# Kernel optimization log

Measured on AMD Instinct MI355X. Metric: run time of the kernel, lower is better.

Reference implementation:

```python
import jax, jax.numpy as jnp
import numpy as np

V, D, NH, T_MAX, L, MLP = 50257, 1024, 16, 1024, 12, 4
HD = D // NH
F = D * MLP
B, T = 2, 1024


def setup_inputs() -> dict:
    key = jax.random.key(0)
    ks = jax.random.split(key, 16)
    s = 0.02
    inp = {
        'tokens': jax.random.randint(ks[0], (B, T), 0, V, dtype=jnp.int32),
        'wte': jax.random.normal(ks[1], (V, D), jnp.float32) * s,
        'wpe': jax.random.normal(ks[2], (T_MAX, D), jnp.float32) * s,
        'ln1_w': jnp.ones((L, D)), 'ln1_b': jnp.zeros((L, D)),
        'attn_w': jax.random.normal(ks[3], (L, D, 3 * D), jnp.float32) * s,
        'attn_b': jnp.zeros((L, 3 * D)),
        'aproj_w': jax.random.normal(ks[4], (L, D, D), jnp.float32) * s,
        'aproj_b': jnp.zeros((L, D)),
        'ln2_w': jnp.ones((L, D)), 'ln2_b': jnp.zeros((L, D)),
        'fc_w': jax.random.normal(ks[5], (L, D, F), jnp.float32) * s,
        'fc_b': jnp.zeros((L, F)),
        'proj_w': jax.random.normal(ks[6], (L, F, D), jnp.float32) * s,
        'proj_b': jnp.zeros((L, D)),
        'lnf_w': jnp.ones((D,)), 'lnf_b': jnp.zeros((D,)),
    }
    return inp


def _ln(x, w, b, eps=1e-5):
    m = jnp.mean(x, -1, keepdims=True)
    v = jnp.var(x, -1, keepdims=True)
    return (x - m) * jax.lax.rsqrt(v + eps) * w + b


def _forward(tokens, wte, wpe, ln1_w, ln1_b, attn_w, attn_b, aproj_w, aproj_b,
             ln2_w, ln2_b, fc_w, fc_b, proj_w, proj_b, lnf_w, lnf_b):
    b, t = tokens.shape
    x = wte[tokens] + wpe[:t]  # [B,T,D]
    scale = HD ** -0.5
    causal = jnp.tril(jnp.ones((t, t), bool))  # [T,T]

    def block(x, p):
        l1w, l1b, aw, ab, apw, apb, l2w, l2b, fw, fb, pw, pb = p
        h = _ln(x, l1w, l1b)
        qkv = h @ aw + ab  # [B,T,3D]
        q, k, v = jnp.split(qkv, 3, axis=-1)
        # rearrange 'b t (h n) -> b n t h' with n=NH: last dim is (head_size, n_heads)
        def split_heads(u):
            return u.reshape(b, t, HD, NH).transpose(0, 3, 1, 2)  # [B,NH,T,HD]
        q, k, v = split_heads(q), split_heads(k), split_heads(v)
        scores = jnp.einsum('bnth,bnsh->bnts', q, k) * scale
        scores = jnp.where(causal, scores, -jnp.inf)
        w = jax.nn.softmax(scores, axis=-1)
        att = jnp.einsum('bnts,bnsh->bnth', w, v)
        # rearrange 'b n t h -> b t (n h)'
        att = att.transpose(0, 2, 1, 3).reshape(b, t, D)
        x = x + (att @ apw + apb)
        h2 = _ln(x, l2w, l2b)
        x = x + (jax.nn.gelu(h2 @ fw + fb, approximate=False) @ pw + pb)
        return x, None

    params = (ln1_w, ln1_b, attn_w, attn_b, aproj_w, aproj_b,
              ln2_w, ln2_b, fc_w, fc_b, proj_w, proj_b)
    x, _ = jax.lax.scan(block, x, params)
    x = _ln(x, lnf_w, lnf_b)[:, -1:, :]  # [B,1,D]
    return x @ wte.T  # tied lm_head -> [B,1,V]


def reference(tokens, wte, wpe, ln1_w, ln1_b, attn_w, attn_b, aproj_w, aproj_b,
              ln2_w, ln2_b, fc_w, fc_b, proj_w, proj_b, lnf_w, lnf_b):
    return _forward(tokens, wte, wpe, ln1_w, ln1_b, attn_w, attn_b, aproj_w,
                    aproj_b, ln2_w, ln2_b, fc_w, fc_b, proj_w, proj_b, lnf_w, lnf_b)
```

## Files before the change

### kernel.cpp

```cpp
#include <hip/hip_runtime.h>
#include <cstdint>
#include <math.h>


using u16 = unsigned short;
using bf16x8 = __attribute__((ext_vector_type(8))) short;
using f32x4 = __attribute__((ext_vector_type(4))) float;

#define GLDS16(g, l)                                                        \
  __builtin_amdgcn_global_load_lds(                                         \
      (const __attribute__((address_space(1))) void*)(g),                   \
      (__attribute__((address_space(3))) void*)(l), 16, 0, 0)

__device__ __forceinline__ u16 f2bf(float f) {
  union { float f; unsigned u; } t; t.f = f;
  unsigned r = t.u + 0x7fffu + ((t.u >> 16) & 1u);
  return (u16)(r >> 16);
}

__device__ __forceinline__ float fast_erf(float x) {
  float ax = fabsf(x);
  float t = 1.f / (1.f + 0.3275911f * ax);
  float y = t * (0.254829592f +
            t * (-0.284496736f +
            t * (1.421413741f +
            t * (-1.453152027f +
            t * 1.061405429f))));
  float r = 1.f - y * __expf(-ax * ax);
  return copysignf(r, x);
}

#define DD 1024
#define TTT 1024
#define MR 2048
#define FFF 4096
#define VVV 50257

__global__ __launch_bounds__(256) void k_embed(const int* __restrict__ tokens,
                                               const float* __restrict__ wte,
                                               const float* __restrict__ wpe,
                                               float* __restrict__ x) {
  int m = blockIdx.x, d = threadIdx.x * 4;
  int t = m & (TTT - 1);
  int tok = tokens[m];
  const float4 a = *(const float4*)(wte + (size_t)tok * DD + d);
  const float4 p = *(const float4*)(wpe + (size_t)t * DD + d);
  float4 o; o.x = a.x + p.x; o.y = a.y + p.y; o.z = a.z + p.z; o.w = a.w + p.w;
  *(float4*)(x + (size_t)m * DD + d) = o;
}

__device__ __forceinline__ void addln_body(float* __restrict__ x,
                                           const float* __restrict__ pp, int npart,
                                           const float* __restrict__ w,
                                           const float* __restrict__ b,
                                           u16* __restrict__ out, int blk) {
  const int wid = threadIdx.x >> 6, lane = threadIdx.x & 63;
  const int m = blk * 4 + wid;
  float* row = x + (size_t)m * DD;
  float4 v[4];
  float s = 0.f, q = 0.f;
#pragma unroll
  for (int j = 0; j < 4; ++j) {
    v[j] = *(const float4*)(row + j * 256 + lane * 4);
    for (int p = 0; p < npart; ++p) {
      const float4 pv = *(const float4*)(pp + (size_t)p * MR * DD + (size_t)m * DD + j * 256 + lane * 4);
      v[j].x += pv.x; v[j].y += pv.y; v[j].z += pv.z; v[j].w += pv.w;
    }
    if (npart) *(float4*)(row + j * 256 + lane * 4) = v[j];
    s += v[j].x + v[j].y + v[j].z + v[j].w;
    q += v[j].x * v[j].x + v[j].y * v[j].y + v[j].z * v[j].z + v[j].w * v[j].w;
  }
#pragma unroll
  for (int off = 1; off < 64; off <<= 1) { s += __shfl_xor(s, off); q += __shfl_xor(q, off); }
  float mean = s * (1.f / DD);
  float var = q * (1.f / DD) - mean * mean;
  float rs = rsqrtf(var + 1e-5f);
#pragma unroll
  for (int j = 0; j < 4; ++j) {
    const float4 wv = *(const float4*)(w + j * 256 + lane * 4);
    const float4 bv = *(const float4*)(b + j * 256 + lane * 4);
    u16 o[4];
    o[0] = f2bf((v[j].x - mean) * rs * wv.x + bv.x);
    o[1] = f2bf((v[j].y - mean) * rs * wv.y + bv.y);
    o[2] = f2bf((v[j].z - mean) * rs * wv.z + bv.z);
    o[3] = f2bf((v[j].w - mean) * rs * wv.w + bv.w);
    *(uint64_t*)(out + (size_t)m * DD + j * 256 + lane * 4) = *(uint64_t*)o;
  }
}

__global__ __launch_bounds__(256) void k_addln(float* __restrict__ x,
                                               const float* __restrict__ pp, int npart,
                                               const float* __restrict__ w,
                                               const float* __restrict__ b,
                                               u16* __restrict__ out) {
  addln_body(x, pp, npart, w, b, out, blockIdx.x);
}

__device__ __forceinline__ void wtrans_body(const float* __restrict__ atw,
                                            const float* __restrict__ apw,
                                            const float* __restrict__ fcw,
                                            const float* __restrict__ pjw,
                                            u16* __restrict__ wt, int id) {
  __shared__ u16 tb[64][72];
  const float* W; u16* Wt; int K, N, local, kts; bool perm = false;
  if (id < 768)       { W = atw; Wt = wt;           K = 1024; N = 3072; local = id;        kts = 4; perm = true; }
  else if (id < 1024) { W = apw; Wt = wt + 3145728; K = 1024; N = 1024; local = id - 768;  kts = 4; }
  else if (id < 2048) { W = fcw; Wt = wt + 4194304; K = 1024; N = 4096; local = id - 1024; kts = 4; }
  else                { W = pjw; Wt = wt + 8388608; K = 4096; N = 1024; local = id - 2048; kts = 6; }
  const int k0 = (local & ((1 << kts) - 1)) * 64, n0 = (local >> kts) * 64;
  const int tid = threadIdx.x;
  const int rr = tid >> 4, c4 = (tid & 15) * 4;
#pragma unroll
  for (int i = 0; i < 4; ++i) {
    const int r = rr + i * 16;
    const float4 v = *(const float4*)(W + (size_t)(k0 + r) * N + n0 + c4);
    tb[c4 + 0][r] = f2bf(v.x);
    tb[c4 + 1][r] = f2bf(v.y);
    tb[c4 + 2][r] = f2bf(v.z);
    tb[c4 + 3][r] = f2bf(v.w);
  }
  __syncthreads();
  const int n = tid >> 3, k8 = (tid & 7) * 8;
#pragma unroll
  for (int s = 0; s < 2; ++s) {
    u16 o[8];
#pragma unroll
    for (int j = 0; j < 8; ++j) o[j] = tb[n + s * 32][k8 + j];
    int orow = n0 + n + s * 32;
    if (perm) {
      int part = orow >> 10, w = orow & 1023;
      orow = part * 1024 + (w & 15) * 64 + (w >> 4);
    }
    *(bf16x8*)(Wt + (size_t)orow * K + k0 + k8) = *(bf16x8*)o;
  }
}

__global__ __launch_bounds__(256) void k_prep(float* __restrict__ x,
                                              const float* __restrict__ pp, int npart,
                                              const float* __restrict__ w,
                                              const float* __restrict__ b,
                                              u16* __restrict__ out,
                                              const float* __restrict__ atw,
                                              const float* __restrict__ apw,
                                              const float* __restrict__ fcw,
                                              const float* __restrict__ pjw,
                                              u16* __restrict__ wt,
                                              const float* __restrict__ ab,
                                              float* __restrict__ pbias) {
  if (blockIdx.x < 512) {
    addln_body(x, pp, npart, w, b, out, blockIdx.x);
  } else if (blockIdx.x == 3584) {
    for (int c = threadIdx.x; c < 3072; c += 256) {
      int part = c >> 10, ww = c & 1023;
      pbias[c] = ab[part * 1024 + (ww & 63) * 16 + (ww >> 6)];
    }
  } else {
    wtrans_body(atw, apw, fcw, pjw, wt, blockIdx.x - 512);
  }
}

template <int EPI>
__global__ __launch_bounds__(256) void k_gemm(const u16* __restrict__ A,
                                              const u16* __restrict__ Bt,
                                              const float* __restrict__ bias,
                                              u16* __restrict__ outb,
                                              float* __restrict__ pp,
                                              int M, int N, int K, int KC) {
  __shared__ u16 As[2][128 * 64];
  __shared__ u16 Bs[2][128 * 64];
  const int nbx = gridDim.x, nby = gridDim.y;
  const int nwg = nbx * nby * gridDim.z;
  const int orig = blockIdx.x + nbx * (blockIdx.y + nby * blockIdx.z);
  const int qq = nwg >> 3, rr = nwg & 7;
  const int xcd = orig & 7, pos = orig >> 3;
  const int wg = (xcd < rr ? xcd * (qq + 1) : rr * (qq + 1) + (xcd - rr) * qq) + pos;
  const int bx = wg % nbx;
  const int tmpw = wg / nbx;
  const int by = tmpw % nby, bz = tmpw / nby;

  const int tid = threadIdx.x;
  const int lane = tid & 63, wid = tid >> 6;
  const int wr = wid >> 1, wc = wid & 1;
  const int l15 = lane & 15, l4 = lane >> 4;
  const int sx = l15 & 7;
  const int m0 = bx * 128, n0 = by * 128;
  f32x4 acc[4][4] = {};

  const int srow = tid >> 3;
  const int scol = (((tid & 7) ^ (srow & 7)) * 8);
  const int k0beg = bz * KC;
  const int nt = KC >> 6;

  const u16* Ap = A + (size_t)(m0 + srow) * K + scol;
  const u16* Bp = Bt + (size_t)(n0 + srow) * K + scol;

#define STAGE(buf, k0)                                                      \
  {                                                                         \
    _Pragma("unroll")                                                       \
    for (int it = 0; it < 4; ++it) {                                        \
      GLDS16(Ap + (size_t)it * 32 * K + (k0), (char*)As[buf] + it * 4096 + tid * 16); \
      GLDS16(Bp + (size_t)it * 32 * K + (k0), (char*)Bs[buf] + it * 4096 + tid * 16); \
    }                                                                       \
  }

  STAGE(0, k0beg);
  for (int t = 0; t < nt; ++t) {
    if (t + 1 < nt) {
      STAGE((t + 1) & 1, k0beg + (t + 1) * 64);
      asm volatile("s_waitcnt vmcnt(8)" ::: "memory");
    } else {
      asm volatile("s_waitcnt vmcnt(0)" ::: "memory");
    }
    __builtin_amdgcn_sched_barrier(0);
    __builtin_amdgcn_s_barrier();
    __builtin_amdgcn_sched_barrier(0);
    const u16* Ab = As[t & 1];
    const u16* Bb = Bs[t & 1];
#pragma unroll
    for (int ks = 0; ks < 2; ++ks) {
      const int ch = ((ks * 4 + l4) ^ sx) * 8;
      bf16x8 af[4], bfr[4];
#pragma unroll
      for (int i = 0; i < 4; ++i)
        af[i] = *(const bf16x8*)(Ab + (wr * 64 + i * 16 + l15) * 64 + ch);
#pragma unroll
      for (int j = 0; j < 4; ++j)
        bfr[j] = *(const bf16x8*)(Bb + (wc * 64 + j * 16 + l15) * 64 + ch);
      __builtin_amdgcn_s_setprio(1);
#pragma unroll
      for (int i = 0; i < 4; ++i)
#pragma unroll
        for (int j = 0; j < 4; ++j)
          acc[i][j] = __builtin_amdgcn_mfma_f32_16x16x32_bf16(af[i], bfr[j], acc[i][j], 0, 0, 0);
      __builtin_amdgcn_s_setprio(0);
    }
    __builtin_amdgcn_sched_barrier(0);
    __builtin_amdgcn_s_barrier();
    __builtin_amdgcn_sched_barrier(0);
  }
#undef STAGE
  float* ppz = (EPI == 4) ? pp + (size_t)bz * M * N : nullptr;
#pragma unroll
  for (int j = 0; j < 4; ++j) {
    const int col = n0 + wc * 64 + j * 16 + l15;
    const float bs = (EPI == 4 && bz != 0) ? 0.f : bias[col];
#pragma unroll
    for (int i = 0; i < 4; ++i) {
#pragma unroll
      for (int r = 0; r < 4; ++r) {
        const int row = m0 + wr * 64 + i * 16 + l4 * 4 + r;
        float v = acc[i][j][r] + bs;
        if (EPI == 0) {
          outb[(size_t)row * N + col] = f2bf(v);
        } else if (EPI == 2) {
          float g = 0.5f * v * (1.f + fast_erf(v * 0.70710678118f));
          outb[(size_t)row * N + col] = f2bf(g);
        } else {
          ppz[(size_t)row * N + col] = v;
        }
      }
    }
  }
}

__global__ __launch_bounds__(256) void k_repack(const u16* __restrict__ qkv,
                                                u16* __restrict__ Vt) {
  __shared__ u16 tile[16][1032];
  const int tid = threadIdx.x;
  const int m0 = blockIdx.x * 16;
  const int b = m0 >> 10;
  const int tg0 = m0 & (TTT - 1);
#pragma unroll
  for (int p = 0; p < 8; ++p) {
    int row = p * 2 + (tid >> 7);
    int col8 = (tid & 127) * 8;
    bf16x8 v = *(const bf16x8*)(qkv + (size_t)(m0 + row) * 3072 + 2048 + col8);
    *(bf16x8*)(&tile[row][col8]) = v;
  }
  __syncthreads();
  const int lane = tid & 63, wid = tid >> 6;
  for (int p = wid; p < 32; p += 4) {
    int n = p >> 1, tc = p & 1;
    u16 o[8];
#pragma unroll
    for (int k = 0; k < 8; ++k) o[k] = tile[tc * 8 + k][n * 64 + lane];
    *(bf16x8*)(Vt + (((size_t)(b * 16 + n)) * 64 + lane) * TTT + tg0 + tc * 8) =
        *(bf16x8*)o;
  }
}

__global__ __launch_bounds__(256) void k_attn(const u16* __restrict__ qkv,
                                              const u16* __restrict__ Vt,
                                              u16* __restrict__ attout) {
  __shared__ u16 Ks[128 * 64];
  __shared__ u16 Vs[64 * 128];
  __shared__ u16 Ps[4][16 * 136];

  const int tid = threadIdx.x;
  const int lane = tid & 63, wid = tid >> 6;
  const int l15 = lane & 15, l4 = lane >> 4;
  const int bn = blockIdx.x;
  const int b = bn >> 4, nh = bn & 15;
  const char* Kg0 = (const char*)(qkv + (size_t)b * TTT * 3072 + 1024 + nh * 64);
  const char* Vg0 = (const char*)(Vt + (size_t)bn * 64 * TTT);

#pragma unroll
  for (int pass = 0; pass < 2; ++pass) {
    const int qtr = pass == 0 ? 15 - (int)blockIdx.y : (int)blockIdx.y;
    const int q0 = qtr * 64;

    const int qrow = q0 + wid * 16 + l15;
    const u16* qsrc = qkv + (size_t)(b * TTT + qrow) * 3072 + nh * 64;
    bf16x8 aq[2];
#pragma unroll
    for (int ks = 0; ks < 2; ++ks)
      aq[ks] = *(const bf16x8*)(qsrc + ks * 32 + l4 * 8);

    float m_run[4], l_part[4];
    f32x4 o[4] = {};
#pragma unroll
    for (int r = 0; r < 4; ++r) { m_run[r] = -1e30f; l_part[r] = 0.f; }

    const int ntk = (qtr >> 1) + 1;
    for (int kt = 0; kt < ntk; ++kt) {
#pragma unroll
      for (int it = 0; it < 4; ++it) {
        int L = it * 4096 + tid * 16;
        int Ls = L ^ (((L >> 7) & 7) << 4);
        int krow = Ls >> 7, cb = Ls & 127;
        GLDS16(Kg0 + (size_t)(kt * 128 + krow) * 6144 + cb, (char*)Ks + L);
      }
#pragma unroll
      for (int it = 0; it < 4; ++it) {
        int L = it * 4096 + tid * 16;
        int Ls = L ^ (((L >> 8) & 7) << 4);
        int hrow = Ls >> 8, cb = Ls & 255;
        GLDS16(Vg0 + (size_t)hrow * 2048 + kt * 256 + cb, (char*)Vs + L);
      }
      __syncthreads();

      f32x4 sf[8];
#pragma unroll
      for (int cf = 0; cf < 8; ++cf) {
        f32x4 z = {};
#pragma unroll
        for (int ks = 0; ks < 2; ++ks) {
          int P = (cf * 16 + l15) * 128 + (ks * 32 + l4 * 8) * 2;
          bf16x8 kb = *(const bf16x8*)((const char*)Ks + (P ^ (((P >> 7) & 7) << 4)));
          z = __builtin_amdgcn_mfma_f32_16x16x32_bf16(aq[ks], kb, z, 0, 0, 0);
        }
        sf[cf] = z;
      }
      const bool lastkt = (kt == ntk - 1);
#pragma unroll
      for (int cf = 0; cf < 8; ++cf)
#pragma unroll
        for (int r = 0; r < 4; ++r) {
          float s = sf[cf][r] * 0.125f;
          if (lastkt) {
            int kg = kt * 128 + cf * 16 + l15;
            int qg = q0 + wid * 16 + l4 * 4 + r;
            if (kg > qg) s = -1e30f;
          }
          sf[cf][r] = s;
        }
      float fac[4];
#pragma unroll
      for (int r = 0; r < 4; ++r) {
        float tm = sf[0][r];
#pragma unroll
        for (int cf = 1; cf < 8; ++cf) tm = fmaxf(tm, sf[cf][r]);
#pragma unroll
        for (int off = 1; off < 16; off <<= 1) tm = fmaxf(tm, __shfl_xor(tm, off));
        float mnew = fmaxf(m_run[r], tm);
        fac[r] = __expf(m_run[r] - mnew);
        m_run[r] = mnew;
        float ps = 0.f;
#pragma unroll
        for (int cf = 0; cf < 8; ++cf) {
          float p = __expf(sf[cf][r] - mnew);
          sf[cf][r] = p;
          ps += p;
        }
        l_part[r] = l_part[r] * fac[r] + ps;
      }
#pragma unroll
      for (int cf = 0; cf < 8; ++cf)
#pragma unroll
        for (int r = 0; r < 4; ++r)
          Ps[wid][(l4 * 4 + r) * 136 + cf * 16 + l15] = f2bf(sf[cf][r]);
#pragma unroll
      for (int hf = 0; hf < 4; ++hf)
#pragma unroll
        for (int r = 0; r < 4; ++r) o[hf][r] *= fac[r];
      bf16x8 pa[4];
#pragma unroll
      for (int ks = 0; ks < 4; ++ks)
        pa[ks] = *(const bf16x8*)&Ps[wid][l15 * 136 + ks * 32 + l4 * 8];
#pragma unroll
      for (int hf = 0; hf < 4; ++hf) {
#pragma unroll
        for (int ks = 0; ks < 4; ++ks) {
          int P = (hf * 16 + l15) * 256 + (ks * 32 + l4 * 8) * 2;
          bf16x8 vb = *(const bf16x8*)((const char*)Vs + (P ^ (((P >> 8) & 7) << 4)));
          o[hf] = __builtin_amdgcn_mfma_f32_16x16x32_bf16(pa[ks], vb, o[hf], 0, 0, 0);
        }
      }
      __syncthreads();
    }
    float lsum[4];
#pragma unroll
    for (int r = 0; r < 4; ++r) {
      float s = l_part[r];
#pragma unroll
      for (int off = 1; off < 16; off <<= 1) s += __shfl_xor(s, off);
      lsum[r] = s;
    }
#pragma unroll
    for (int hf = 0; hf < 4; ++hf)
#pragma unroll
      for (int r = 0; r < 4; ++r) {
        float val = o[hf][r] / lsum[r];
        size_t row = (size_t)b * TTT + q0 + wid * 16 + l4 * 4 + r;
        attout[row * DD + nh * 64 + hf * 16 + l15] = f2bf(val);
      }
  }
}

__global__ __launch_bounds__(256) void k_head(const float* __restrict__ x,
                                              const float* __restrict__ pp, int npart,
                                              const float* __restrict__ lnf_w,
                                              const float* __restrict__ lnf_b,
                                              const float* __restrict__ wte,
                                              float* __restrict__ out) {
  __shared__ float xs[2 * DD];
  __shared__ float sm[8];
  int tid = threadIdx.x;
  int wid = tid >> 6, lane = tid & 63;
#pragma unroll
  for (int bb = 0; bb < 2; ++bb) {
    int m = bb * TTT + (TTT - 1);
    float4 v = *(const float4*)(x + (size_t)m * DD + tid * 4);
    for (int p = 0; p < npart; ++p) {
      const float4 pv = *(const float4*)(pp + (size_t)p * MR * DD + (size_t)m * DD + tid * 4);
      v.x += pv.x; v.y += pv.y; v.z += pv.z; v.w += pv.w;
    }
    float s = v.x + v.y + v.z + v.w;
    float q = v.x * v.x + v.y * v.y + v.z * v.z + v.w * v.w;
#pragma unroll
    for (int off = 1; off < 64; off <<= 1) { s += __shfl_xor(s, off); q += __shfl_xor(q, off); }
    if ((tid & 63) == 0) { sm[wid] = s; sm[4 + wid] = q; }
    __syncthreads();
    s = sm[0] + sm[1] + sm[2] + sm[3];
    q = sm[4] + sm[5] + sm[6] + sm[7];
    float mean = s * (1.f / DD);
    float var = q * (1.f / DD) - mean * mean;
    float rs = rsqrtf(var + 1e-5f);
    const float4 wv = *(const float4*)(lnf_w + tid * 4);
    const float4 bv = *(const float4*)(lnf_b + tid * 4);
    float4 o;
    o.x = (v.x - mean) * rs * wv.x + bv.x;
    o.y = (v.y - mean) * rs * wv.y + bv.y;
    o.z = (v.z - mean) * rs * wv.z + bv.z;
    o.w = (v.w - mean) * rs * wv.w + bv.w;
    *(float4*)(xs + bb * DD + tid * 4) = o;
    __syncthreads();
  }
  for (int v = blockIdx.x * 4 + wid; v < VVV; v += gridDim.x * 4) {
    const float* wr = wte + (size_t)v * DD;
    float a0 = 0.f, a1 = 0.f;
#pragma unroll
    for (int j = 0; j < 4; ++j) {
      const float4 wv = *(const float4*)(wr + lane * 16 + j * 4);
      const float4 x0 = *(const float4*)(xs + lane * 16 + j * 4);
      const float4 x1 = *(const float4*)(xs + DD + lane * 16 + j * 4);
      a0 += wv.x * x0.x + wv.y * x0.y + wv.z * x0.z + wv.w * x0.w;
      a1 += wv.x * x1.x + wv.y * x1.y + wv.z * x1.z + wv.w * x1.w;
    }
#pragma unroll
    for (int off = 1; off < 64; off <<= 1) { a0 += __shfl_xor(a0, off); a1 += __shfl_xor(a1, off); }
    if (lane == 0) { out[v] = a0; out[VVV + v] = a1; }
  }
}

extern "C" void kernel_launch(void* const* d_in, const int* in_sizes, int n_in,
                              void* d_out, int out_size, void* d_ws, size_t ws_size,
                              hipStream_t stream) {
  const int* tokens    = (const int*)d_in[0];
  const float* wte     = (const float*)d_in[1];
  const float* wpe     = (const float*)d_in[2];
  const float* ln1_w   = (const float*)d_in[3];
  const float* ln1_b   = (const float*)d_in[4];
  const float* attn_w  = (const float*)d_in[5];
  const float* attn_b  = (const float*)d_in[6];
  const float* aproj_w = (const float*)d_in[7];
  const float* aproj_b = (const float*)d_in[8];
  const float* ln2_w   = (const float*)d_in[9];
  const float* ln2_b   = (const float*)d_in[10];
  const float* fc_w    = (const float*)d_in[11];
  const float* fc_b    = (const float*)d_in[12];
  const float* proj_w  = (const float*)d_in[13];
  const float* proj_b  = (const float*)d_in[14];
  const float* lnf_w   = (const float*)d_in[15];
  const float* lnf_b   = (const float*)d_in[16];

  char* ws = (char*)d_ws;
  float* x    = (float*)(ws);
  u16* h      = (u16*)(ws + (8u << 20));
  u16* wt     = (u16*)(ws + (12u << 20));
  u16* qkv    = (u16*)(ws + (36u << 20));
  u16* Vt     = (u16*)(ws + (52u << 20));
  u16* attb   = (u16*)(ws + (56u << 20));
  u16* mlph   = (u16*)(ws + (36u << 20));
  float* pp   = (float*)(ws + (60u << 20));
  float* pbias = (float*)(ws + (92u << 20));
  float* out  = (float*)d_out;

  u16* atw = wt;
  u16* apw = wt + 3145728;
  u16* fcw = wt + 4194304;
  u16* pjw = wt + 8388608;

  k_embed<<<MR, 256, 0, stream>>>(tokens, wte, wpe, x);

  for (int l = 0; l < 12; ++l) {
    k_prep<<<3585, 256, 0, stream>>>(x, pp, l == 0 ? 0 : 4,
                                     ln1_w + l * DD, ln1_b + l * DD, h,
                                     attn_w + (size_t)l * DD * 3 * DD,
                                     aproj_w + (size_t)l * DD * DD,
                                     fc_w + (size_t)l * DD * FFF,
                                     proj_w + (size_t)l * FFF * DD, wt,
                                     attn_b + (size_t)l * 3 * DD, pbias);
    k_gemm<0><<<dim3(16, 24, 1), 256, 0, stream>>>(h, atw, pbias, qkv, nullptr, MR, 3072, 1024, 1024);
    k_repack<<<128, 256, 0, stream>>>(qkv, Vt);
    k_attn<<<dim3(32, 8), 256, 0, stream>>>(qkv, Vt, attb);
    k_gemm<4><<<dim3(16, 8, 2), 256, 0, stream>>>(attb, apw, aproj_b + (size_t)l * DD, nullptr, pp, MR, 1024, 1024, 512);
    k_addln<<<512, 256, 0, stream>>>(x, pp, 2, ln2_w + l * DD, ln2_b + l * DD, h);
    k_gemm<2><<<dim3(16, 32, 1), 256, 0, stream>>>(h, fcw, fc_b + (size_t)l * FFF, mlph, nullptr, MR, 4096, 1024, 1024);
    k_gemm<4><<<dim3(16, 8, 4), 256, 0, stream>>>(mlph, pjw, proj_b + (size_t)l * DD, nullptr, pp, MR, 1024, 4096, 1024);
  }
  k_head<<<512, 256, 0, stream>>>(x, pp, 4, lnf_w, lnf_b, wte, out);
}
```

Before: 1.857 ms.

## Stage GEMM epilogue through LDS, store split-K partials as bf16

The GEMM epilogue now writes results into shared memory and then emits coalesced 16-byte row stores, replacing scattered per-element global writes. Split-K partial sums are stored as bf16 instead of fp32, halving partial-buffer traffic in the GEMM and the add+layernorm consumers. The attention projection is split four ways instead of two. Storing partials in bf16 loses precision in the residual accumulation, and the extra split adds partial traffic.

```diff
diff --git a/kernel.cpp b/kernel.cpp
--- a/kernel.cpp
+++ b/kernel.cpp
@@ -16,6 +16,10 @@
   union { float f; unsigned u; } t; t.f = f;
   unsigned r = t.u + 0x7fffu + ((t.u >> 16) & 1u);
   return (u16)(r >> 16);
+}
+__device__ __forceinline__ float bf2f(u16 v) {
+  union { unsigned u; float f; } t; t.u = ((unsigned)v) << 16;
+  return t.f;
 }
 
 __device__ __forceinline__ float fast_erf(float x) {
@@ -50,7 +54,7 @@
 }
 
 __device__ __forceinline__ void addln_body(float* __restrict__ x,
-                                           const float* __restrict__ pp, int npart,
+                                           const u16* __restrict__ pp, int npart,
                                            const float* __restrict__ w,
                                            const float* __restrict__ b,
                                            u16* __restrict__ out, int blk) {
@@ -62,9 +66,13 @@
 #pragma unroll
   for (int j = 0; j < 4; ++j) {
     v[j] = *(const float4*)(row + j * 256 + lane * 4);
+#pragma unroll 4
     for (int p = 0; p < npart; ++p) {
-      const float4 pv = *(const float4*)(pp + (size_t)p * MR * DD + (size_t)m * DD + j * 256 + lane * 4);
-      v[j].x += pv.x; v[j].y += pv.y; v[j].z += pv.z; v[j].w += pv.w;
+      uint64_t pv = *(const uint64_t*)(pp + (size_t)p * MR * DD + (size_t)m * DD + j * 256 + lane * 4);
+      v[j].x += bf2f((u16)(pv));
+      v[j].y += bf2f((u16)(pv >> 16));
+      v[j].z += bf2f((u16)(pv >> 32));
+      v[j].w += bf2f((u16)(pv >> 48));
     }
     if (npart) *(float4*)(row + j * 256 + lane * 4) = v[j];
     s += v[j].x + v[j].y + v[j].z + v[j].w;
@@ -89,7 +97,7 @@
 }
 
 __global__ __launch_bounds__(256) void k_addln(float* __restrict__ x,
-                                               const float* __restrict__ pp, int npart,
+                                               const u16* __restrict__ pp, int npart,
                                                const float* __restrict__ w,
                                                const float* __restrict__ b,
                                                u16* __restrict__ out) {
@@ -136,7 +144,7 @@
 }
 
 __global__ __launch_bounds__(256) void k_prep(float* __restrict__ x,
-                                              const float* __restrict__ pp, int npart,
+                                              const u16* __restrict__ pp, int npart,
                                               const float* __restrict__ w,
                                               const float* __restrict__ b,
                                               u16* __restrict__ out,
@@ -164,10 +172,9 @@
                                               const u16* __restrict__ Bt,
                                               const float* __restrict__ bias,
                                               u16* __restrict__ outb,
-                                              float* __restrict__ pp,
+                                              u16* __restrict__ pp,
                                               int M, int N, int K, int KC) {
-  __shared__ u16 As[2][128 * 64];
-  __shared__ u16 Bs[2][128 * 64];
+  __shared__ u16 smem[4][128 * 64];
   const int nbx = gridDim.x, nby = gridDim.y;
   const int nwg = nbx * nby * gridDim.z;
   const int orig = blockIdx.x + nbx * (blockIdx.y + nby * blockIdx.z);
@@ -198,8 +205,8 @@
   {                                                                         \
     _Pragma("unroll")                                                       \
     for (int it = 0; it < 4; ++it) {                                        \
-      GLDS16(Ap + (size_t)it * 32 * K + (k0), (char*)As[buf] + it * 4096 + tid * 16); \
-      GLDS16(Bp + (size_t)it * 32 * K + (k0), (char*)Bs[buf] + it * 4096 + tid * 16); \
+      GLDS16(Ap + (size_t)it * 32 * K + (k0), (char*)smem[buf] + it * 4096 + tid * 16); \
+      GLDS16(Bp + (size_t)it * 32 * K + (k0), (char*)smem[2 + (buf)] + it * 4096 + tid * 16); \
     }                                                                       \
   }
 
@@ -214,8 +221,8 @@
     __builtin_amdgcn_sched_barrier(0);
     __builtin_amdgcn_s_barrier();
     __builtin_amdgcn_sched_barrier(0);
-    const u16* Ab = As[t & 1];
-    const u16* Bb = Bs[t & 1];
+    const u16* Ab = smem[t & 1];
+    const u16* Bb = smem[2 + (t & 1)];
 #pragma unroll
     for (int ks = 0; ks < 2; ++ks) {
       const int ch = ((ks * 4 + l4) ^ sx) * 8;
@@ -239,28 +246,31 @@
     __builtin_amdgcn_sched_barrier(0);
   }
 #undef STAGE
-  float* ppz = (EPI == 4) ? pp + (size_t)bz * M * N : nullptr;
+  u16* eb = (u16*)smem;
 #pragma unroll
   for (int j = 0; j < 4; ++j) {
-    const int col = n0 + wc * 64 + j * 16 + l15;
-    const float bs = (EPI == 4 && bz != 0) ? 0.f : bias[col];
+    const int col = wc * 64 + j * 16 + l15;
+    const float bs = (EPI == 4 && bz != 0) ? 0.f : bias[n0 + col];
 #pragma unroll
     for (int i = 0; i < 4; ++i) {
 #pragma unroll
       for (int r = 0; r < 4; ++r) {
-        const int row = m0 + wr * 64 + i * 16 + l4 * 4 + r;
+        const int row = wr * 64 + i * 16 + l4 * 4 + r;
         float v = acc[i][j][r] + bs;
-        if (EPI == 0) {
-          outb[(size_t)row * N + col] = f2bf(v);
-        } else if (EPI == 2) {
-          float g = 0.5f * v * (1.f + fast_erf(v * 0.70710678118f));
-          outb[(size_t)row * N + col] = f2bf(g);
-        } else {
-          ppz[(size_t)row * N + col] = v;
-        }
-      }
-    }
-  }
+        if (EPI == 2) v = 0.5f * v * (1.f + fast_erf(v * 0.70710678118f));
+        eb[row * 132 + col] = f2bf(v);
+      }
+    }
+  }
+  __syncthreads();
+  const int erow = tid >> 1;
+  const int ecol0 = (tid & 1) * 64;
+  u16* gout = (EPI == 4) ? (pp + (size_t)bz * M * N) : outb;
+  u16* gdst = gout + (size_t)(m0 + erow) * N + n0 + ecol0;
+  const u16* esrc = eb + erow * 132 + ecol0;
+#pragma unroll
+  for (int c = 0; c < 8; ++c)
+    *(bf16x8*)(gdst + c * 8) = *(const bf16x8*)(esrc + c * 8);
 }
 
 __global__ __launch_bounds__(256) void k_repack(const u16* __restrict__ qkv,
@@ -428,7 +438,7 @@
 }
 
 __global__ __launch_bounds__(256) void k_head(const float* __restrict__ x,
-                                              const float* __restrict__ pp, int npart,
+                                              const u16* __restrict__ pp, int npart,
                                               const float* __restrict__ lnf_w,
                                               const float* __restrict__ lnf_b,
                                               const float* __restrict__ wte,
@@ -441,9 +451,13 @@
   for (int bb = 0; bb < 2; ++bb) {
     int m = bb * TTT + (TTT - 1);
     float4 v = *(const float4*)(x + (size_t)m * DD + tid * 4);
+#pragma unroll 4
     for (int p = 0; p < npart; ++p) {
-      const float4 pv = *(const float4*)(pp + (size_t)p * MR * DD + (size_t)m * DD + tid * 4);
-      v.x += pv.x; v.y += pv.y; v.z += pv.z; v.w += pv.w;
+      uint64_t pv = *(const uint64_t*)(pp + (size_t)p * MR * DD + (size_t)m * DD + tid * 4);
+      v.x += bf2f((u16)(pv));
+      v.y += bf2f((u16)(pv >> 16));
+      v.z += bf2f((u16)(pv >> 32));
+      v.w += bf2f((u16)(pv >> 48));
     }
     float s = v.x + v.y + v.z + v.w;
     float q = v.x * v.x + v.y * v.y + v.z * v.z + v.w * v.w;
@@ -512,7 +526,7 @@
   u16* Vt     = (u16*)(ws + (52u << 20));
   u16* attb   = (u16*)(ws + (56u << 20));
   u16* mlph   = (u16*)(ws + (36u << 20));
-  float* pp   = (float*)(ws + (60u << 20));
+  u16* pp     = (u16*)(ws + (60u << 20));
   float* pbias = (float*)(ws + (92u << 20));
   float* out  = (float*)d_out;
 
@@ -534,8 +548,8 @@
     k_gemm<0><<<dim3(16, 24, 1), 256, 0, stream>>>(h, atw, pbias, qkv, nullptr, MR, 3072, 1024, 1024);
     k_repack<<<128, 256, 0, stream>>>(qkv, Vt);
     k_attn<<<dim3(32, 8), 256, 0, stream>>>(qkv, Vt, attb);
-    k_gemm<4><<<dim3(16, 8, 2), 256, 0, stream>>>(attb, apw, aproj_b + (size_t)l * DD, nullptr, pp, MR, 1024, 1024, 512);
-    k_addln<<<512, 256, 0, stream>>>(x, pp, 2, ln2_w + l * DD, ln2_b + l * DD, h);
+    k_gemm<4><<<dim3(16, 8, 4), 256, 0, stream>>>(attb, apw, aproj_b + (size_t)l * DD, nullptr, pp, MR, 1024, 1024, 256);
+    k_addln<<<512, 256, 0, stream>>>(x, pp, 4, ln2_w + l * DD, ln2_b + l * DD, h);
     k_gemm<2><<<dim3(16, 32, 1), 256, 0, stream>>>(h, fcw, fc_b + (size_t)l * FFF, mlph, nullptr, MR, 4096, 1024, 1024);
     k_gemm<4><<<dim3(16, 8, 4), 256, 0, stream>>>(mlph, pjw, proj_b + (size_t)l * DD, nullptr, pp, MR, 1024, 4096, 1024);
   }
```

New measurement: 1.837 ms. Within noise of the previous version (-1.0%).
